# Kernel optimization log

Measured on AMD Instinct MI355X. Metric: run time of the kernel, lower is better.

Reference implementation:

```python
import jax, jax.numpy as jnp
import numpy as np

D_MODEL = 256
N_HEAD = 4
HEAD_DIM = D_MODEL // N_HEAD  # 64


def setup_inputs() -> dict:
    key = jax.random.key(0)
    kx, kw, kb = jax.random.split(key, 3)
    x = jax.random.normal(kx, (4, 2048, D_MODEL), dtype=jnp.float32)
    # nn.Linear(256, 768): weight [768, 256], bias [768]
    bound = 1.0 / np.sqrt(D_MODEL)
    W_qkv = jax.random.uniform(kw, (3 * D_MODEL, D_MODEL), dtype=jnp.float32, minval=-bound, maxval=bound)
    b_qkv = jax.random.uniform(kb, (3 * D_MODEL,), dtype=jnp.float32, minval=-bound, maxval=bound)
    return {"x": x, "W_qkv": W_qkv, "b_qkv": b_qkv}


def reference(x, W_qkv, b_qkv):
    B, S, _ = x.shape
    # fused QKV projection: [B, S, 3*D]
    qkv = jnp.einsum("bsd,ed->bse", x, W_qkv) + b_qkv
    q, k, v = jnp.split(qkv, 3, axis=-1)
    # [B, S, D] -> [B, H, S, Dh]
    def to_heads(t):
        return t.reshape(B, S, N_HEAD, HEAD_DIM).transpose(0, 2, 1, 3)
    q, k, v = to_heads(q), to_heads(k), to_heads(v)
    scale = 1.0 / np.sqrt(HEAD_DIM)
    # scores [B, H, S, S]
    scores = jnp.einsum("bhqd,bhkd->bhqk", q, k) * scale
    attn = jax.nn.softmax(scores, axis=-1)
    out = jnp.einsum("bhqk,bhkd->bhqd", attn, v)  # [B, H, S, Dh]
    return out
```

## Files before the change

kernel.cpp:

```cpp
#include <hip/hip_runtime.h>

#define BB 4
#define SS 2048
#define DM 256
#define NH 4
#define DH 64
#define NROW (BB*SS)
#define NE   (3*DM)
#define BH   (BB*NH)
#define HEAD_ELEMS (BH*SS*DH)
#define NQROWS (BH*SS)

typedef _Float16 half_t;
typedef __attribute__((ext_vector_type(8))) _Float16 half8;
typedef __attribute__((ext_vector_type(4))) _Float16 half4;
typedef __attribute__((ext_vector_type(4))) float floatx4;

#define KPAD 72

#define QK_SCALE 0.18033688011112042f
#define EXP2(x) __builtin_amdgcn_exp2f(x)
#define DEFER_THR 8.0f

__global__ __launch_bounds__(256) void prep(const float* __restrict__ x,
                                            const float* __restrict__ W,
                                            half_t* __restrict__ xh,
                                            half_t* __restrict__ xl,
                                            half_t* __restrict__ wh) {
    int gtid = blockIdx.x * 256 + threadIdx.x;
    {
        int i = gtid * 4;
        float4 v = *(const float4*)&x[i];
        half4 h, l;
        h.x = (half_t)v.x; l.x = (half_t)(v.x - (float)h.x);
        h.y = (half_t)v.y; l.y = (half_t)(v.y - (float)h.y);
        h.z = (half_t)v.z; l.z = (half_t)(v.z - (float)h.z);
        h.w = (half_t)v.w; l.w = (half_t)(v.w - (float)h.w);
        *(half4*)&xh[i] = h;
        *(half4*)&xl[i] = l;
    }
    if (gtid < NE * DM / 4) {
        int i = gtid * 4;
        float4 v = *(const float4*)&W[i];
        half4 h;
        h.x = (half_t)v.x; h.y = (half_t)v.y;
        h.z = (half_t)v.z; h.w = (half_t)v.w;
        *(half4*)&wh[i] = h;
    }
}

__global__ __launch_bounds__(256) void qkv_proj(const half_t* __restrict__ xh,
                                                const half_t* __restrict__ xl,
                                                const half_t* __restrict__ whg,
                                                const float* __restrict__ bias,
                                                half_t* __restrict__ qh,
                                                half_t* __restrict__ kh,
                                                half_t* __restrict__ vt) {
    __shared__ __align__(16) half_t Xh[64 * KPAD];
    __shared__ __align__(16) half_t Xl[64 * KPAD];
    __shared__ __align__(16) half_t Wh[64 * KPAD];

    const int rb   = blockIdx.x * 64;
    const int nb   = blockIdx.y * 64;
    const int tid  = threadIdx.x;
    const int wid  = tid >> 6;
    const int lane = tid & 63;
    const int quad = lane >> 4;
    const int col  = lane & 15;

    floatx4 acc[4];
    #pragma unroll
    for (int t = 0; t < 4; ++t) acc[t] = (floatx4){0.f, 0.f, 0.f, 0.f};

    for (int k0 = 0; k0 < DM; k0 += 64) {
        __syncthreads();
        #pragma unroll
        for (int i = 0; i < 2; ++i) {
            int gi = tid + 256 * i;
            int r  = gi >> 3;
            int c8 = (gi & 7) * 8;
            *(half8*)&Xh[r * KPAD + c8] = *(const half8*)&xh[(size_t)(rb + r) * DM + k0 + c8];
            *(half8*)&Xl[r * KPAD + c8] = *(const half8*)&xl[(size_t)(rb + r) * DM + k0 + c8];
            *(half8*)&Wh[r * KPAD + c8] = *(const half8*)&whg[(size_t)(nb + r) * DM + k0 + c8];
        }
        __syncthreads();

        half8 ah0 = *(const half8*)&Xh[(wid * 16 + col) * KPAD + quad * 8];
        half8 ah1 = *(const half8*)&Xh[(wid * 16 + col) * KPAD + 32 + quad * 8];
        half8 al0 = *(const half8*)&Xl[(wid * 16 + col) * KPAD + quad * 8];
        half8 al1 = *(const half8*)&Xl[(wid * 16 + col) * KPAD + 32 + quad * 8];

        #pragma unroll
        for (int t = 0; t < 4; ++t) {
            half8 bh0 = *(const half8*)&Wh[(t * 16 + col) * KPAD + quad * 8];
            half8 bh1 = *(const half8*)&Wh[(t * 16 + col) * KPAD + 32 + quad * 8];
            acc[t] = __builtin_amdgcn_mfma_f32_16x16x32_f16(ah0, bh0, acc[t], 0, 0, 0);
            acc[t] = __builtin_amdgcn_mfma_f32_16x16x32_f16(ah1, bh1, acc[t], 0, 0, 0);
            acc[t] = __builtin_amdgcn_mfma_f32_16x16x32_f16(al0, bh0, acc[t], 0, 0, 0);
            acc[t] = __builtin_amdgcn_mfma_f32_16x16x32_f16(al1, bh1, acc[t], 0, 0, 0);
        }
    }

    const int part = nb >> 8;
    const int mloc = wid * 16 + quad * 4;
    if (part != 2) {
        #pragma unroll
        for (int t = 0; t < 4; ++t) {
            int e    = nb + t * 16 + col;
            float be = bias[e];
            int dm   = e & 255;
            int h    = dm >> 6;
            int dh   = dm & 63;
            #pragma unroll
            for (int r = 0; r < 4; ++r) {
                int row = rb + mloc + r;
                int b   = row >> 11;
                int s   = row & 2047;
                int bh_ = b * NH + h;
                float val = acc[t][r] + be;
                if (part == 0) {
                    qh[((size_t)bh_ * SS + s) * DH + dh] = (half_t)(val * QK_SCALE);
                } else {
                    kh[((size_t)bh_ * SS + s) * DH + dh] = (half_t)val;
                }
            }
        }
    } else {
        __syncthreads();
        #pragma unroll
        for (int t = 0; t < 4; ++t) {
            int e    = nb + t * 16 + col;
            float be = bias[e];
            #pragma unroll
            for (int r = 0; r < 4; ++r)
                Xh[(t * 16 + col) * KPAD + mloc + r] = (half_t)(acc[t][r] + be);
        }
        __syncthreads();
        const int b   = rb >> 11;
        const int s0  = rb & 2047;
        const int h   = (nb >> 6) & 3;
        const int bh_ = b * NH + h;
        #pragma unroll
        for (int i = 0; i < 2; ++i) {
            int idx = tid + 256 * i;
            int rr  = idx >> 3;
            int cc8 = (idx & 7) * 8;
            *(half8*)&vt[((size_t)bh_ * DH + rr) * SS + s0 + cc8] =
                *(const half8*)&Xh[rr * KPAD + cc8];
        }
    }
}

__global__ __launch_bounds__(256, 4) void attn(const half_t* __restrict__ qh,
                                               const half_t* __restrict__ kh,
                                               const half_t* __restrict__ vt,
                                               half_t* __restrict__ pO,
                                               float* __restrict__ mst,
                                               float* __restrict__ lst) {
    __shared__ __align__(16) half_t Ks[64 * KPAD];
    __shared__ __align__(16) half_t Vts[64 * KPAD];

    const int q0   = blockIdx.x * 64;
    const int bh   = blockIdx.y;
    const int kz   = blockIdx.z;
    const size_t base = (size_t)bh * SS * DH;
    const int tid  = threadIdx.x;
    const int wid  = tid >> 6;
    const int lane = tid & 63;
    const int quad = lane >> 4;
    const int col  = lane & 15;
    const int ktBeg = kz * (SS / 2);
    const int ktEnd = ktBeg + (SS / 2);

    int srr[2], scc[2];
    #pragma unroll
    for (int i = 0; i < 2; ++i) {
        int gi = tid + 256 * i;
        srr[i] = gi >> 3;
        scc[i] = (gi & 7) * 8;
    }

    half8 bq0, bq1;
    {
        int s = q0 + wid * 16 + col;
        bq0 = *(const half8*)&qh[base + (size_t)s * DH + quad * 8];
        bq1 = *(const half8*)&qh[base + (size_t)s * DH + 32 + quad * 8];
    }

    half8 ck[2], cv[2], nk[2], nv[2];
    #pragma unroll
    for (int i = 0; i < 2; ++i) {
        ck[i] = *(const half8*)&kh[base + (size_t)(ktBeg + srr[i]) * DH + scc[i]];
        cv[i] = *(const half8*)&vt[base + (size_t)srr[i] * SS + ktBeg + scc[i]];
        nk[i] = ck[i];
        nv[i] = cv[i];
    }

    float m_i = -3.0e38f;
    float l_i = 0.f;
    floatx4 o[4];
    #pragma unroll
    for (int dt = 0; dt < 4; ++dt) o[dt] = (floatx4){0.f, 0.f, 0.f, 0.f};

    for (int kt = ktBeg; kt < ktEnd; kt += 64) {
        __syncthreads();
        #pragma unroll
        for (int i = 0; i < 2; ++i) {
            *(half8*)&Ks[srr[i] * KPAD + scc[i]]  = ck[i];
            *(half8*)&Vts[srr[i] * KPAD + scc[i]] = cv[i];
        }
        __syncthreads();

        const int ktn = kt + 64;
        if (ktn < ktEnd) {
            #pragma unroll
            for (int i = 0; i < 2; ++i) {
                nk[i] = *(const half8*)&kh[base + (size_t)(ktn + srr[i]) * DH + scc[i]];
                nv[i] = *(const half8*)&vt[base + (size_t)srr[i] * SS + ktn + scc[i]];
            }
        }

        floatx4 sc[4];
        #pragma unroll
        for (int t = 0; t < 4; ++t) {
            half8 ak0 = *(const half8*)&Ks[(t * 16 + col) * KPAD + quad * 8];
            half8 ak1 = *(const half8*)&Ks[(t * 16 + col) * KPAD + 32 + quad * 8];
            floatx4 c = (floatx4){0.f, 0.f, 0.f, 0.f};
            c = __builtin_amdgcn_mfma_f32_16x16x32_f16(ak0, bq0, c, 0, 0, 0);
            c = __builtin_amdgcn_mfma_f32_16x16x32_f16(ak1, bq1, c, 0, 0, 0);
            sc[t] = c;
        }

        float mloc = -3.0e38f;
        #pragma unroll
        for (int t = 0; t < 4; ++t) {
            float a = fmaxf(fmaxf(sc[t][0], sc[t][1]), fmaxf(sc[t][2], sc[t][3]));
            mloc = fmaxf(mloc, a);
        }
        mloc = fmaxf(mloc, __shfl_xor(mloc, 16));
        mloc = fmaxf(mloc, __shfl_xor(mloc, 32));

        bool skip = __all(mloc <= m_i + DEFER_THR);
        float m_new = skip ? m_i : fmaxf(m_i, mloc);

        half4 pa[4];
        float rsum = 0.f;
        #pragma unroll
        for (int t = 0; t < 4; ++t) {
            float p0 = EXP2(sc[t][0] - m_new);
            float p1 = EXP2(sc[t][1] - m_new);
            float p2 = EXP2(sc[t][2] - m_new);
            float p3 = EXP2(sc[t][3] - m_new);
            rsum += p0 + p1 + p2 + p3;
            pa[t] = (half4){(half_t)p0, (half_t)p1, (half_t)p2, (half_t)p3};
        }
        rsum += __shfl_xor(rsum, 16);
        rsum += __shfl_xor(rsum, 32);

        if (skip) {
            l_i += rsum;
        } else {
            float alpha = EXP2(m_i - m_new);
            m_i = m_new;
            l_i = l_i * alpha + rsum;
            float ar[4];
            #pragma unroll
            for (int i = 0; i < 4; ++i) ar[i] = __shfl(alpha, quad * 4 + i);
            #pragma unroll
            for (int dt = 0; dt < 4; ++dt)
                #pragma unroll
                for (int i = 0; i < 4; ++i)
                    o[dt][i] *= ar[i];
        }

        #pragma unroll
        for (int t = 0; t < 4; ++t) {
            #pragma unroll
            for (int dt = 0; dt < 4; ++dt) {
                half4 bv = *(const half4*)&Vts[(dt * 16 + col) * KPAD + t * 16 + quad * 4];
                o[dt] = __builtin_amdgcn_mfma_f32_16x16x16f16(pa[t], bv, o[dt], 0, 0, 0);
            }
        }

        #pragma unroll
        for (int i = 0; i < 2; ++i) { ck[i] = nk[i]; cv[i] = nv[i]; }
    }

    const size_t pbase = (size_t)kz * HEAD_ELEMS + base;
    {
        float inv = 1.0f / l_i;
        float ir[4];
        #pragma unroll
        for (int i = 0; i < 4; ++i) ir[i] = __shfl(inv, quad * 4 + i);
        #pragma unroll
        for (int dt = 0; dt < 4; ++dt)
            #pragma unroll
            for (int i = 0; i < 4; ++i) {
                int row = q0 + wid * 16 + quad * 4 + i;
                pO[pbase + (size_t)row * DH + dt * 16 + col] = (half_t)(o[dt][i] * ir[i]);
            }
        if (quad == 0) {
            int row = q0 + wid * 16 + col;
            int idx = kz * NQROWS + bh * SS + row;
            mst[idx] = m_i;
            lst[idx] = l_i;
        }
    }
}

__global__ __launch_bounds__(256) void merge(const half_t* __restrict__ pO,
                                             const float* __restrict__ mst,
                                             const float* __restrict__ lst,
                                             float* __restrict__ out) {
    int gid = blockIdx.x * 256 + threadIdx.x;
    int row = gid >> 3;
    int dc  = (gid & 7) * 8;
    float m1 = mst[row], m2 = mst[NQROWS + row];
    float l1 = lst[row], l2 = lst[NQROWS + row];
    float M  = fmaxf(m1, m2);
    float w1 = l1 * EXP2(m1 - M);
    float w2 = l2 * EXP2(m2 - M);
    float inv = 1.0f / (w1 + w2);
    float a = w1 * inv, b = w2 * inv;
    half8 o1 = *(const half8*)&pO[(size_t)row * DH + dc];
    half8 o2 = *(const half8*)&pO[(size_t)HEAD_ELEMS + (size_t)row * DH + dc];
    float4 r0, r1;
    r0.x = a * (float)o1[0] + b * (float)o2[0];
    r0.y = a * (float)o1[1] + b * (float)o2[1];
    r0.z = a * (float)o1[2] + b * (float)o2[2];
    r0.w = a * (float)o1[3] + b * (float)o2[3];
    r1.x = a * (float)o1[4] + b * (float)o2[4];
    r1.y = a * (float)o1[5] + b * (float)o2[5];
    r1.z = a * (float)o1[6] + b * (float)o2[6];
    r1.w = a * (float)o1[7] + b * (float)o2[7];
    *(float4*)&out[(size_t)row * DH + dc]     = r0;
    *(float4*)&out[(size_t)row * DH + dc + 4] = r1;
}

extern "C" void kernel_launch(void* const* d_in, const int* in_sizes, int n_in,
                              void* d_out, int out_size, void* d_ws, size_t ws_size,
                              hipStream_t stream) {
    const float* x  = (const float*)d_in[0];
    const float* Wq = (const float*)d_in[1];
    const float* bq = (const float*)d_in[2];
    float* out = (float*)d_out;

    half_t* qh  = (half_t*)d_ws;
    half_t* kh  = qh + (size_t)HEAD_ELEMS;
    half_t* vt  = kh + (size_t)HEAD_ELEMS;
    half_t* xh  = vt + (size_t)HEAD_ELEMS;
    half_t* xl  = xh + (size_t)HEAD_ELEMS;
    half_t* whp = xl + (size_t)HEAD_ELEMS;
    half_t* pO  = xh;
    float*  mst = (float*)((char*)d_ws + 21364736);
    float*  lst = mst + 2 * NQROWS;

    prep<<<2048, 256, 0, stream>>>(x, Wq, xh, xl, whp);
    qkv_proj<<<dim3(NROW / 64, NE / 64), 256, 0, stream>>>(xh, xl, whp, bq, qh, kh, vt);
    attn<<<dim3(SS / 64, BH, 2), 256, 0, stream>>>(qh, kh, vt, pO, mst, lst);
    merge<<<1024, 256, 0, stream>>>(pO, mst, lst, out);
}
```

Measured before the change: 118.8 us.

## Shrink attention blocks to 32 queries, remap blocks per XCD, defer row-sum reduction

The attention kernel now launches 128-thread blocks covering 32 query rows, doubling the block count. Block indices are remapped so blocks sharing the same (batch-head, key-half) stream land on the same XCD, which is meant to improve L2 reuse of K/V tiles. The per-iteration cross-lane reduction of the softmax row sum is moved out of the loop, and the duplicate current/next prefetch registers are merged into a single set. Each thread now loads twice as many K/V chunks into shared memory per tile. Total K/V traffic per query roughly doubles because fewer queries share each loaded tile.

New measurement: 123.3 us. 3.8% more time.

```diff
diff --git a/kernel.cpp b/kernel.cpp
--- a/kernel.cpp
+++ b/kernel.cpp
@@ -151,7 +151,7 @@
     }
 }
 
-__global__ __launch_bounds__(256, 4) void attn(const half_t* __restrict__ qh,
+__global__ __launch_bounds__(128, 4) void attn(const half_t* __restrict__ qh,
                                                const half_t* __restrict__ kh,
                                                const half_t* __restrict__ vt,
                                                half_t* __restrict__ pO,
@@ -160,9 +160,14 @@
     __shared__ __align__(16) half_t Ks[64 * KPAD];
     __shared__ __align__(16) half_t Vts[64 * KPAD];
 
-    const int q0   = blockIdx.x * 64;
-    const int bh   = blockIdx.y;
-    const int kz   = blockIdx.z;
+    const int lin  = blockIdx.x + 64 * blockIdx.y + 1024 * blockIdx.z;
+    const int xcd  = lin & 7;
+    const int j    = lin >> 3;
+    const int strm = xcd + 8 * (j >> 6);
+    const int q0   = (j & 63) * 32;
+    const int bh   = strm & 15;
+    const int kz   = strm >> 4;
+
     const size_t base = (size_t)bh * SS * DH;
     const int tid  = threadIdx.x;
     const int wid  = tid >> 6;
@@ -172,10 +177,10 @@
     const int ktBeg = kz * (SS / 2);
     const int ktEnd = ktBeg + (SS / 2);
 
-    int srr[2], scc[2];
+    int srr[4], scc[4];
     #pragma unroll
-    for (int i = 0; i < 2; ++i) {
-        int gi = tid + 256 * i;
+    for (int i = 0; i < 4; ++i) {
+        int gi = tid + 128 * i;
         srr[i] = gi >> 3;
         scc[i] = (gi & 7) * 8;
     }
@@ -187,17 +192,15 @@
         bq1 = *(const half8*)&qh[base + (size_t)s * DH + 32 + quad * 8];
     }
 
-    half8 ck[2], cv[2], nk[2], nv[2];
+    half8 nk[4], nv[4];
     #pragma unroll
-    for (int i = 0; i < 2; ++i) {
-        ck[i] = *(const half8*)&kh[base + (size_t)(ktBeg + srr[i]) * DH + scc[i]];
-        cv[i] = *(const half8*)&vt[base + (size_t)srr[i] * SS + ktBeg + scc[i]];
-        nk[i] = ck[i];
-        nv[i] = cv[i];
+    for (int i = 0; i < 4; ++i) {
+        nk[i] = *(const half8*)&kh[base + (size_t)(ktBeg + srr[i]) * DH + scc[i]];
+        nv[i] = *(const half8*)&vt[base + (size_t)srr[i] * SS + ktBeg + scc[i]];
     }
 
     float m_i = -3.0e38f;
-    float l_i = 0.f;
+    float l_part = 0.f;
     floatx4 o[4];
     #pragma unroll
     for (int dt = 0; dt < 4; ++dt) o[dt] = (floatx4){0.f, 0.f, 0.f, 0.f};
@@ -205,16 +208,16 @@
     for (int kt = ktBeg; kt < ktEnd; kt += 64) {
         __syncthreads();
         #pragma unroll
-        for (int i = 0; i < 2; ++i) {
-            *(half8*)&Ks[srr[i] * KPAD + scc[i]]  = ck[i];
-            *(half8*)&Vts[srr[i] * KPAD + scc[i]] = cv[i];
+        for (int i = 0; i < 4; ++i) {
+            *(half8*)&Ks[srr[i] * KPAD + scc[i]]  = nk[i];
+            *(half8*)&Vts[srr[i] * KPAD + scc[i]] = nv[i];
         }
         __syncthreads();
 
         const int ktn = kt + 64;
         if (ktn < ktEnd) {
             #pragma unroll
-            for (int i = 0; i < 2; ++i) {
+            for (int i = 0; i < 4; ++i) {
                 nk[i] = *(const half8*)&kh[base + (size_t)(ktn + srr[i]) * DH + scc[i]];
                 nv[i] = *(const half8*)&vt[base + (size_t)srr[i] * SS + ktn + scc[i]];
             }
@@ -244,25 +247,23 @@
         float m_new = skip ? m_i : fmaxf(m_i, mloc);
 
         half4 pa[4];
-        float rsum = 0.f;
+        float rsumL = 0.f;
         #pragma unroll
         for (int t = 0; t < 4; ++t) {
             float p0 = EXP2(sc[t][0] - m_new);
             float p1 = EXP2(sc[t][1] - m_new);
             float p2 = EXP2(sc[t][2] - m_new);
             float p3 = EXP2(sc[t][3] - m_new);
-            rsum += p0 + p1 + p2 + p3;
+            rsumL += p0 + p1 + p2 + p3;
             pa[t] = (half4){(half_t)p0, (half_t)p1, (half_t)p2, (half_t)p3};
         }
-        rsum += __shfl_xor(rsum, 16);
-        rsum += __shfl_xor(rsum, 32);
 
         if (skip) {
-            l_i += rsum;
+            l_part += rsumL;
         } else {
             float alpha = EXP2(m_i - m_new);
             m_i = m_new;
-            l_i = l_i * alpha + rsum;
+            l_part = l_part * alpha + rsumL;
             float ar[4];
             #pragma unroll
             for (int i = 0; i < 4; ++i) ar[i] = __shfl(alpha, quad * 4 + i);
@@ -281,10 +282,10 @@
                 o[dt] = __builtin_amdgcn_mfma_f32_16x16x16f16(pa[t], bv, o[dt], 0, 0, 0);
             }
         }
-
-        #pragma unroll
-        for (int i = 0; i < 2; ++i) { ck[i] = nk[i]; cv[i] = nv[i]; }
-    }
+    }
+
+    float l_i = l_part + __shfl_xor(l_part, 16);
+    l_i += __shfl_xor(l_i, 32);
 
     const size_t pbase = (size_t)kz * HEAD_ELEMS + base;
     {
@@ -357,6 +358,6 @@
 
     prep<<<2048, 256, 0, stream>>>(x, Wq, xh, xl, whp);
     qkv_proj<<<dim3(NROW / 64, NE / 64), 256, 0, stream>>>(xh, xl, whp, bq, qh, kh, vt);
-    attn<<<dim3(SS / 64, BH, 2), 256, 0, stream>>>(qh, kh, vt, pO, mst, lst);
+    attn<<<dim3(SS / 32, BH, 2), 128, 0, stream>>>(qh, kh, vt, pO, mst, lst);
     merge<<<1024, 256, 0, stream>>>(pO, mst, lst, out);
 }
```
